# Kernel tuning notes

Measured on AMD Instinct MI355X. Metric: run time of the kernel, lower is better.

Reference implementation:

```python
import jax, jax.numpy as jnp
import numpy as np

THRESHOLD = 1.5
MIN_AREA = 3
B, H, W = 8, 1024, 1024


def _label_components(mask):
    """8-connectivity connected-component labeling by min-index propagation.
    mask: [B,H,W] bool. Returns int32 labels [B,H,W]; each component is labeled
    by the minimum global flat index of its pixels; background pixels = B*H*W.
    Labels are globally unique across the batch (matches sort_labels' per-batch
    unique relabeling up to a label permutation).
    """
    N = B * H * W
    SENT = jnp.int32(N)
    flat = jnp.arange(N, dtype=jnp.int32).reshape(B, H, W)
    lab0 = jnp.where(mask, flat, SENT)

    def neighbor_min(lab):
        p = jnp.pad(lab, ((0, 0), (1, 1), (1, 1)), constant_values=N)
        m = lab
        for dr in (-1, 0, 1):
            for dc in (-1, 0, 1):
                if dr == 0 and dc == 0:
                    continue
                m = jnp.minimum(m, p[:, 1 + dr:1 + dr + H, 1 + dc:1 + dc + W])
        return jnp.where(mask, m, SENT)

    def cond(state):
        return state[1]

    def body(state):
        lab, _ = state
        new = neighbor_min(lab)
        return new, jnp.any(new != lab)

    lab, _ = jax.lax.while_loop(cond, body, (lab0, jnp.array(True)))
    return lab


def setup_inputs() -> dict:
    key = jax.random.key(0)
    x = jax.random.normal(key, (B, H, W // 1), dtype=jnp.float32)
    return {"input_tensor": x.reshape(B, 1, H, W)}


def reference(input_tensor):
    """Dense encoding of the original ragged output: for every pixel belonging
    to a cluster with area > MIN_AREA, emit the cluster's max value and the
    (row, col) of the first (lowest flat index) occurrence of that max;
    background / small-cluster pixels get (0, -1, -1). Since THRESHOLD > 0,
    max over masked_fill(0) in the original equals max over cluster pixels.
    """
    x = input_tensor[:, 0]                  # [B,H,W]
    N = B * H * W
    nseg = N + 1                            # last segment = background
    mask = (x >= THRESHOLD)
    ids = _label_components(mask).reshape(-1)          # [N] int32 in [0, N]
    vals = x.reshape(-1)
    fg = mask.reshape(-1)

    area = jax.ops.segment_sum(fg.astype(jnp.float32), ids, num_segments=nseg)
    cmax = jax.ops.segment_max(vals, ids, num_segments=nseg)

    within = jnp.tile(jnp.arange(H * W, dtype=jnp.int32), B)  # flat idx in image
    is_max = (vals == cmax[ids]) & fg
    cand = jnp.where(is_max, within, jnp.int32(H * W))
    amin = jax.ops.segment_min(cand, ids, num_segments=nseg)  # first argmax

    valid = fg & (area[ids] > MIN_AREA)
    out_max = jnp.where(valid, cmax[ids], jnp.float32(0.0)).reshape(B, H, W)
    aidx = amin[ids]
    row = jnp.where(valid, aidx // W, jnp.int32(-1)).reshape(B, H, W)
    col = jnp.where(valid, aidx % W, jnp.int32(-1)).reshape(B, H, W)
    return out_max, row, col
```

## Files before the change

kernel.cpp:

```cpp
#include <hip/hip_runtime.h>
#include <stdint.h>

#define THRESH 1.5f
constexpr int NPIX  = 8 * 1024 * 1024;
constexpr int HW    = 1024 * 1024;
constexpr int WW    = 1024;
constexpr int NWORD = NPIX / 32;
constexpr int WPR   = WW / 32;

constexpr int BLK     = 256;
constexpr int GRD_PX4 = NPIX / (BLK * 4);
constexpr int GRD_W   = NWORD / BLK;

constexpr int SPB_R      = 128;
constexpr int BASE_SLOTS = GRD_PX4 * SPB_R;
constexpr int OVF_SLOTS  = 16384;
constexpr int CAP        = BASE_SLOTS + OVF_SLOTS;
constexpr int ZINT4 = CAP * 12 / 16;
static_assert((CAP * 12) % 16 == 0, "zero region must be int4-divisible");
static_assert(ZINT4 <= GRD_PX4 * BLK, "mask_init must cover the zero region");

constexpr int WLSTRIDE = 1024;


__device__ __forceinline__ int find_root(int* __restrict__ P, int x) {
    int p = P[x];
    while (p != x) {
        int g = P[p];
        if (g != p) P[x] = g;
        x = p; p = g;
    }
    return x;
}

__device__ __forceinline__ void merge(int* P, int a, int b) {
    int ra = find_root(P, a);
    int rb = find_root(P, b);
    while (ra != rb) {
        if (ra < rb) { int t = ra; ra = rb; rb = t; }
        int old = atomicCAS(&P[ra], ra, rb);
        if (old == ra) break;
        ra = find_root(P, old);
        rb = find_root(P, rb);
    }
}

__global__ void mask_init_k(const float* __restrict__ x, int* __restrict__ parent,
                            unsigned* __restrict__ mask, uint2* __restrict__ wl,
                            int* __restrict__ wl_cnt, int4* __restrict__ zbase,
                            int* __restrict__ ovf) {
    __shared__ unsigned s_nib[BLK];
    __shared__ unsigned s_word[WPR];
    __shared__ int s_rank;
    int t  = threadIdx.x;
    int gt = blockIdx.x * BLK + t;
    if (gt < ZINT4) zbase[gt] = make_int4(0, 0, 0, 0);
    int i4 = gt * 4;
    float4 v = *(const float4*)(x + i4);
    unsigned nib = (unsigned)(v.x >= THRESH) | ((unsigned)(v.y >= THRESH) << 1) |
                   ((unsigned)(v.z >= THRESH) << 2) | ((unsigned)(v.w >= THRESH) << 3);
    if (t == 0) s_rank = 0;
    s_nib[t] = nib;
    __syncthreads();
    if ((t & 7) == 0) {
        unsigned w = 0;
        #pragma unroll
        for (int k = 0; k < 8; k++) w |= s_nib[t + k] << (4 * k);
        s_word[t >> 3] = w;
        mask[gt >> 3] = w;
    }
    __syncthreads();

    int rowstart = blockIdx.x << 10;
    int r0 = t << 2;
    int rs0 = 0, rs1 = 0, rs2 = 0, rs3 = 0;
    if (nib & 1u) {
        bool prevSet = (r0 != 0) &&
            ((s_word[(r0 - 1) >> 5] >> ((r0 - 1) & 31)) & 1u);
        if (!prevSet) rs0 = r0;
        else {
            int wI = r0 >> 5, b = r0 & 31;
            unsigned notset = b ? (~s_word[wI] & ((1u << b) - 1)) : 0u;
            int j = wI;
            if (!notset) {
                j = wI - 1;
                while (j >= 0 && s_word[j] == 0xFFFFFFFFu) j--;
                notset = (j >= 0) ? ~s_word[j] : 0u;
            }
            rs0 = (j < 0) ? 0 : (j * 32 + (31 - __clz(notset)) + 1);
        }
    }
    if (nib & 2u) rs1 = (nib & 1u) ? rs0 : r0 + 1;
    if (nib & 4u) rs2 = (nib & 2u) ? rs1 : r0 + 2;
    if (nib & 8u) rs3 = (nib & 4u) ? rs2 : r0 + 3;
    int4 pv;
    pv.x = (nib & 1u) ? rowstart + rs0 : i4;
    pv.y = (nib & 2u) ? rowstart + rs1 : i4 + 1;
    pv.z = (nib & 4u) ? rowstart + rs2 : i4 + 2;
    pv.w = (nib & 8u) ? rowstart + rs3 : i4 + 3;
    *(int4*)(parent + i4) = pv;

    int nfg = __popc(nib);
    if (nfg) {
        int r = atomicAdd(&s_rank, nfg);
        uint2* dst = wl + (size_t)blockIdx.x * WLSTRIDE;
        if (nib & 1u) dst[r++] = make_uint2((unsigned)i4,     __float_as_uint(v.x));
        if (nib & 2u) dst[r++] = make_uint2((unsigned)i4 + 1, __float_as_uint(v.y));
        if (nib & 4u) dst[r++] = make_uint2((unsigned)i4 + 2, __float_as_uint(v.z));
        if (nib & 8u) dst[r++] = make_uint2((unsigned)i4 + 3, __float_as_uint(v.w));
    }
    __syncthreads();
    if (t == 0) wl_cnt[blockIdx.x] = s_rank;
    if (gt == 0) *ovf = 0;
}

__global__ void union_k(const unsigned* __restrict__ mask, int* __restrict__ parent) {
    int w = blockIdx.x * BLK + threadIdx.x;
    int r = (w >> 5) & (WW - 1);
    if (r == 0) return;
    unsigned cur = mask[w];
    if (!cur) return;
    int cw = w & (WPR - 1);
    unsigned above     = mask[w - WPR];
    unsigned abovePrev = (cw > 0)       ? mask[w - WPR - 1] : 0u;
    unsigned aboveNext = (cw < WPR - 1) ? mask[w - WPR + 1] : 0u;
    unsigned mN  = cur & above;
    unsigned mNW = cur & ((above << 1) | (abovePrev >> 31));
    unsigned mNE = cur & ((above >> 1) | ((aboveNext & 1u) << 31));
    mNW &= ~mN;
    mNE &= ~mN;
    mN  &= ~(mN << 1);
    if (!(mN | mNW | mNE)) return;
    int base = w << 5;
    while (mN)  { int b = __ffs(mN)  - 1; mN  &= mN  - 1; merge(parent, base + b, base + b - WW); }
    while (mNW) { int b = __ffs(mNW) - 1; mNW &= mNW - 1; merge(parent, base + b, base + b - WW - 1); }
    while (mNE) { int b = __ffs(mNE) - 1; mNE &= mNE - 1; merge(parent, base + b, base + b - WW + 1); }
}

__global__ void cstats_k(const uint2* __restrict__ wl, const int* __restrict__ wl_cnt,
                         int* __restrict__ parent, int* __restrict__ cnt,
                         unsigned long long* __restrict__ best,
                         int* __restrict__ ovf) {
    __shared__ int s_cnt;
    if (threadIdx.x == 0) s_cnt = 0;
    __syncthreads();
    int region = blockIdx.x;
    int c = wl_cnt[region];
    const uint2* src = wl + (size_t)region * WLSTRIDE;
    for (int j = threadIdx.x; j < c; j += 64) {
        uint2 e = src[j];
        int p = (int)e.x;
        int cid;
        int xn = p;
        while (true) {
            int pe = parent[xn];
            if (pe >= NPIX) { cid = pe - NPIX; break; }
            if (pe == xn) {
                int rank = atomicAdd(&s_cnt, 1);
                int slot;
                if (rank < SPB_R) slot = region * SPB_R + rank;
                else { int o2 = atomicAdd(ovf, 1);
                       slot = BASE_SLOTS + (o2 < OVF_SLOTS ? o2 : OVF_SLOTS - 1); }
                int old = atomicCAS(&parent[xn], xn, NPIX + slot);
                if (old == xn)    { cid = slot; break; }
                if (old >= NPIX)  { cid = old - NPIX; break; }
                xn = old;
            } else {
                xn = pe;
            }
        }
        parent[p] = NPIX + cid;
        atomicAdd(&cnt[cid], 1);
        unsigned within = (unsigned)(p & (HW - 1));
        unsigned long long pk =
            ((unsigned long long)e.y << 32) | (unsigned long long)(~within);
        atomicMax(&best[cid], pk);
    }
}

__device__ __forceinline__ void lookup_one(const int* __restrict__ parent,
                                           const int* __restrict__ cnt,
                                           const unsigned long long* __restrict__ best,
                                           int p, float& om, float& orow, float& ocol) {
    int cid = parent[p] - NPIX;
    if (cid >= 0 && cid < CAP && cnt[cid] > 3) {
        unsigned long long pk = best[cid];
        om   = __uint_as_float((unsigned)(pk >> 32));
        unsigned idx = ~((unsigned)pk);
        orow = (float)(idx >> 10);
        ocol = (float)(idx & (WW - 1));
    }
}

__global__ void out_k(const unsigned* __restrict__ mask, const int* __restrict__ parent,
                      const int* __restrict__ cnt,
                      const unsigned long long* __restrict__ best,
                      float* __restrict__ o) {
    int t = blockIdx.x * BLK + threadIdx.x;
    unsigned nib = (mask[t >> 3] >> ((t & 7) * 4)) & 0xFu;
    int i4 = t * 4;
    float4 m  = make_float4(0.f, 0.f, 0.f, 0.f);
    float4 rr = make_float4(-1.f, -1.f, -1.f, -1.f);
    float4 cc = make_float4(-1.f, -1.f, -1.f, -1.f);
    if (nib) {
        if (nib & 1u) lookup_one(parent, cnt, best, i4,     m.x, rr.x, cc.x);
        if (nib & 2u) lookup_one(parent, cnt, best, i4 + 1, m.y, rr.y, cc.y);
        if (nib & 4u) lookup_one(parent, cnt, best, i4 + 2, m.z, rr.z, cc.z);
        if (nib & 8u) lookup_one(parent, cnt, best, i4 + 3, m.w, rr.w, cc.w);
    }
    *(float4*)(o + i4)            = m;
    *(float4*)(o + NPIX + i4)     = rr;
    *(float4*)(o + 2 * NPIX + i4) = cc;
}

extern "C" void kernel_launch(void* const* d_in, const int* in_sizes, int n_in,
                              void* d_out, int out_size, void* d_ws, size_t ws_size,
                              hipStream_t stream) {
    const float* x = (const float*)d_in[0];
    float* o = (float*)d_out;

    char* base = (char*)d_ws;
    int* parent = (int*)base;
    size_t off = (size_t)NPIX * 4;
    unsigned long long* best = (unsigned long long*)(base + off);
    int4* zbase = (int4*)(base + off);                             off += (size_t)CAP * 8;
    int* cnt       = (int*)(base + off);                           off += (size_t)CAP * 4;
    unsigned* mask = (unsigned*)(base + off);                      off += (size_t)NWORD * 4;
    int* wl_cnt    = (int*)(base + off);                           off += (size_t)GRD_PX4 * 4;
    uint2* wl      = (uint2*)(base + off);                         off += (size_t)GRD_PX4 * WLSTRIDE * 8;
    int* ovf       = (int*)(base + off);

    mask_init_k<<<GRD_PX4, BLK, 0, stream>>>(x, parent, mask, wl, wl_cnt, zbase, ovf);
    union_k    <<<GRD_W,   BLK, 0, stream>>>(mask, parent);
    cstats_k   <<<GRD_PX4, 64,  0, stream>>>(wl, wl_cnt, parent, cnt, best, ovf);
    out_k      <<<GRD_PX4, BLK, 0, stream>>>(mask, parent, cnt, best, o);
}
```

Measured before the change: 189.7 us.

## Write default outputs in mask init and scatter cluster stats via worklist

The background default values (0,-1,-1) are now written in the first kernel while it already streams the input. The final full-image output pass is replaced by a sparse kernel that walks each block's foreground worklist and scatters stats only for foreground pixels. The cluster id is stored back into the worklist instead of parent, and parent writes are skipped for background-only threads. This removes a full read of mask and parent plus a dense gather pass, at the cost of scattered scalar stores and a 64-thread sparse launch.

```diff
diff --git a/kernel.cpp b/kernel.cpp
--- a/kernel.cpp
+++ b/kernel.cpp
@@ -48,7 +48,7 @@
 __global__ void mask_init_k(const float* __restrict__ x, int* __restrict__ parent,
                             unsigned* __restrict__ mask, uint2* __restrict__ wl,
                             int* __restrict__ wl_cnt, int4* __restrict__ zbase,
-                            int* __restrict__ ovf) {
+                            int* __restrict__ ovf, float* __restrict__ o) {
     __shared__ unsigned s_nib[BLK];
     __shared__ unsigned s_word[WPR];
     __shared__ int s_rank;
@@ -59,6 +59,10 @@
     float4 v = *(const float4*)(x + i4);
     unsigned nib = (unsigned)(v.x >= THRESH) | ((unsigned)(v.y >= THRESH) << 1) |
                    ((unsigned)(v.z >= THRESH) << 2) | ((unsigned)(v.w >= THRESH) << 3);
+    const float4 neg1 = make_float4(-1.f, -1.f, -1.f, -1.f);
+    *(float4*)(o + i4)            = make_float4(0.f, 0.f, 0.f, 0.f);
+    *(float4*)(o + NPIX + i4)     = neg1;
+    *(float4*)(o + 2 * NPIX + i4) = neg1;
     if (t == 0) s_rank = 0;
     s_nib[t] = nib;
     __syncthreads();
@@ -71,37 +75,37 @@
     }
     __syncthreads();
 
-    int rowstart = blockIdx.x << 10;
-    int r0 = t << 2;
-    int rs0 = 0, rs1 = 0, rs2 = 0, rs3 = 0;
-    if (nib & 1u) {
-        bool prevSet = (r0 != 0) &&
-            ((s_word[(r0 - 1) >> 5] >> ((r0 - 1) & 31)) & 1u);
-        if (!prevSet) rs0 = r0;
-        else {
-            int wI = r0 >> 5, b = r0 & 31;
-            unsigned notset = b ? (~s_word[wI] & ((1u << b) - 1)) : 0u;
-            int j = wI;
-            if (!notset) {
-                j = wI - 1;
-                while (j >= 0 && s_word[j] == 0xFFFFFFFFu) j--;
-                notset = (j >= 0) ? ~s_word[j] : 0u;
+    if (nib) {
+        int rowstart = blockIdx.x << 10;
+        int r0 = t << 2;
+        int rs0 = 0, rs1 = 0, rs2 = 0, rs3 = 0;
+        if (nib & 1u) {
+            bool prevSet = (r0 != 0) &&
+                ((s_word[(r0 - 1) >> 5] >> ((r0 - 1) & 31)) & 1u);
+            if (!prevSet) rs0 = r0;
+            else {
+                int wI = r0 >> 5, b = r0 & 31;
+                unsigned notset = b ? (~s_word[wI] & ((1u << b) - 1)) : 0u;
+                int j = wI;
+                if (!notset) {
+                    j = wI - 1;
+                    while (j >= 0 && s_word[j] == 0xFFFFFFFFu) j--;
+                    notset = (j >= 0) ? ~s_word[j] : 0u;
+                }
+                rs0 = (j < 0) ? 0 : (j * 32 + (31 - __clz(notset)) + 1);
             }
-            rs0 = (j < 0) ? 0 : (j * 32 + (31 - __clz(notset)) + 1);
         }
-    }
-    if (nib & 2u) rs1 = (nib & 1u) ? rs0 : r0 + 1;
-    if (nib & 4u) rs2 = (nib & 2u) ? rs1 : r0 + 2;
-    if (nib & 8u) rs3 = (nib & 4u) ? rs2 : r0 + 3;
-    int4 pv;
-    pv.x = (nib & 1u) ? rowstart + rs0 : i4;
-    pv.y = (nib & 2u) ? rowstart + rs1 : i4 + 1;
-    pv.z = (nib & 4u) ? rowstart + rs2 : i4 + 2;
-    pv.w = (nib & 8u) ? rowstart + rs3 : i4 + 3;
-    *(int4*)(parent + i4) = pv;
-
-    int nfg = __popc(nib);
-    if (nfg) {
+        if (nib & 2u) rs1 = (nib & 1u) ? rs0 : r0 + 1;
+        if (nib & 4u) rs2 = (nib & 2u) ? rs1 : r0 + 2;
+        if (nib & 8u) rs3 = (nib & 4u) ? rs2 : r0 + 3;
+        int4 pv;
+        pv.x = (nib & 1u) ? rowstart + rs0 : i4;
+        pv.y = (nib & 2u) ? rowstart + rs1 : i4 + 1;
+        pv.z = (nib & 4u) ? rowstart + rs2 : i4 + 2;
+        pv.w = (nib & 8u) ? rowstart + rs3 : i4 + 3;
+        *(int4*)(parent + i4) = pv;
+
+        int nfg = __popc(nib);
         int r = atomicAdd(&s_rank, nfg);
         uint2* dst = wl + (size_t)blockIdx.x * WLSTRIDE;
         if (nib & 1u) dst[r++] = make_uint2((unsigned)i4,     __float_as_uint(v.x));
@@ -137,7 +141,7 @@
     while (mNE) { int b = __ffs(mNE) - 1; mNE &= mNE - 1; merge(parent, base + b, base + b - WW + 1); }
 }
 
-__global__ void cstats_k(const uint2* __restrict__ wl, const int* __restrict__ wl_cnt,
+__global__ void cstats_k(uint2* __restrict__ wl, const int* __restrict__ wl_cnt,
                          int* __restrict__ parent, int* __restrict__ cnt,
                          unsigned long long* __restrict__ best,
                          int* __restrict__ ovf) {
@@ -146,7 +150,7 @@
     __syncthreads();
     int region = blockIdx.x;
     int c = wl_cnt[region];
-    const uint2* src = wl + (size_t)region * WLSTRIDE;
+    uint2* src = wl + (size_t)region * WLSTRIDE;
     for (int j = threadIdx.x; j < c; j += 64) {
         uint2 e = src[j];
         int p = (int)e.x;
@@ -169,7 +173,7 @@
                 xn = pe;
             }
         }
-        parent[p] = NPIX + cid;
+        src[j] = make_uint2(e.x, (unsigned)cid);
         atomicAdd(&cnt[cid], 1);
         unsigned within = (unsigned)(p & (HW - 1));
         unsigned long long pk =
@@ -178,39 +182,26 @@
     }
 }
 
-__device__ __forceinline__ void lookup_one(const int* __restrict__ parent,
-                                           const int* __restrict__ cnt,
-                                           const unsigned long long* __restrict__ best,
-                                           int p, float& om, float& orow, float& ocol) {
-    int cid = parent[p] - NPIX;
-    if (cid >= 0 && cid < CAP && cnt[cid] > 3) {
-        unsigned long long pk = best[cid];
-        om   = __uint_as_float((unsigned)(pk >> 32));
-        unsigned idx = ~((unsigned)pk);
-        orow = (float)(idx >> 10);
-        ocol = (float)(idx & (WW - 1));
-    }
-}
-
-__global__ void out_k(const unsigned* __restrict__ mask, const int* __restrict__ parent,
-                      const int* __restrict__ cnt,
-                      const unsigned long long* __restrict__ best,
-                      float* __restrict__ o) {
-    int t = blockIdx.x * BLK + threadIdx.x;
-    unsigned nib = (mask[t >> 3] >> ((t & 7) * 4)) & 0xFu;
-    int i4 = t * 4;
-    float4 m  = make_float4(0.f, 0.f, 0.f, 0.f);
-    float4 rr = make_float4(-1.f, -1.f, -1.f, -1.f);
-    float4 cc = make_float4(-1.f, -1.f, -1.f, -1.f);
-    if (nib) {
-        if (nib & 1u) lookup_one(parent, cnt, best, i4,     m.x, rr.x, cc.x);
-        if (nib & 2u) lookup_one(parent, cnt, best, i4 + 1, m.y, rr.y, cc.y);
-        if (nib & 4u) lookup_one(parent, cnt, best, i4 + 2, m.z, rr.z, cc.z);
-        if (nib & 8u) lookup_one(parent, cnt, best, i4 + 3, m.w, rr.w, cc.w);
-    }
-    *(float4*)(o + i4)            = m;
-    *(float4*)(o + NPIX + i4)     = rr;
-    *(float4*)(o + 2 * NPIX + i4) = cc;
+__global__ void sval_k(const uint2* __restrict__ wl, const int* __restrict__ wl_cnt,
+                       const int* __restrict__ cnt,
+                       const unsigned long long* __restrict__ best,
+                       float* __restrict__ o) {
+    int region = blockIdx.x;
+    int c = wl_cnt[region];
+    const uint2* src = wl + (size_t)region * WLSTRIDE;
+    for (int j = threadIdx.x; j < c; j += 64) {
+        uint2 e = src[j];
+        int p   = (int)e.x;
+        int cid = (int)e.y;
+        if (cid < 0 || cid >= CAP) continue;
+        if (cnt[cid] > 3) {
+            unsigned long long pk = best[cid];
+            unsigned idx = ~((unsigned)pk);
+            o[p]            = __uint_as_float((unsigned)(pk >> 32));
+            o[NPIX + p]     = (float)(idx >> 10);
+            o[2 * NPIX + p] = (float)(idx & (WW - 1));
+        }
+    }
 }
 
 extern "C" void kernel_launch(void* const* d_in, const int* in_sizes, int n_in,
@@ -230,8 +221,8 @@
     uint2* wl      = (uint2*)(base + off);                         off += (size_t)GRD_PX4 * WLSTRIDE * 8;
     int* ovf       = (int*)(base + off);
 
-    mask_init_k<<<GRD_PX4, BLK, 0, stream>>>(x, parent, mask, wl, wl_cnt, zbase, ovf);
+    mask_init_k<<<GRD_PX4, BLK, 0, stream>>>(x, parent, mask, wl, wl_cnt, zbase, ovf, o);
     union_k    <<<GRD_W,   BLK, 0, stream>>>(mask, parent);
     cstats_k   <<<GRD_PX4, 64,  0, stream>>>(wl, wl_cnt, parent, cnt, best, ovf);
-    out_k      <<<GRD_PX4, BLK, 0, stream>>>(mask, parent, cnt, best, o);
-}
+    sval_k     <<<GRD_PX4, 64,  0, stream>>>(wl, wl_cnt, cnt, best, o);
+}
```

New measurement: 197.3 us. 4.0% more time.

## Fuse intra-stripe row unions into mask init, union only stripe boundaries

Applied to the files above, without the earlier changes.

The mask/init kernel now processes 8-row stripes per block, keeps the stripe's bitmask words in shared memory, and performs the vertical unions between rows inside the stripe directly. A separate lightweight kernel then unions only the first row of each stripe with the row above. cstats now packs four 64-thread wavefronts per block, each handling one row region. This cuts global mask re-reads and launch work for the union pass, but gives fewer, longer-running blocks in the init kernel, with many barriers per block.

```diff
diff --git a/kernel.cpp b/kernel.cpp
--- a/kernel.cpp
+++ b/kernel.cpp
@@ -8,17 +8,19 @@
 constexpr int NWORD = NPIX / 32;
 constexpr int WPR   = WW / 32;
 
-constexpr int BLK     = 256;
-constexpr int GRD_PX4 = NPIX / (BLK * 4);
-constexpr int GRD_W   = NWORD / BLK;
+constexpr int BLK      = 256;
+constexpr int NROWS    = NPIX / WW;
+constexpr int SROWS    = 8;
+constexpr int NSTRIPE  = NROWS / SROWS;
+constexpr int GRD_PX4  = NPIX / (BLK * 4);
+constexpr int GRD_BU   = (NSTRIPE * WPR) / BLK;
 
 constexpr int SPB_R      = 128;
-constexpr int BASE_SLOTS = GRD_PX4 * SPB_R;
+constexpr int BASE_SLOTS = NROWS * SPB_R;
 constexpr int OVF_SLOTS  = 16384;
 constexpr int CAP        = BASE_SLOTS + OVF_SLOTS;
 constexpr int ZINT4 = CAP * 12 / 16;
 static_assert((CAP * 12) % 16 == 0, "zero region must be int4-divisible");
-static_assert(ZINT4 <= GRD_PX4 * BLK, "mask_init must cover the zero region");
 
 constexpr int WLSTRIDE = 1024;
 
@@ -45,109 +47,135 @@
     }
 }
 
-__global__ void mask_init_k(const float* __restrict__ x, int* __restrict__ parent,
-                            unsigned* __restrict__ mask, uint2* __restrict__ wl,
-                            int* __restrict__ wl_cnt, int4* __restrict__ zbase,
-                            int* __restrict__ ovf) {
-    __shared__ unsigned s_nib[BLK];
-    __shared__ unsigned s_word[WPR];
-    __shared__ int s_rank;
-    int t  = threadIdx.x;
-    int gt = blockIdx.x * BLK + t;
-    if (gt < ZINT4) zbase[gt] = make_int4(0, 0, 0, 0);
-    int i4 = gt * 4;
-    float4 v = *(const float4*)(x + i4);
-    unsigned nib = (unsigned)(v.x >= THRESH) | ((unsigned)(v.y >= THRESH) << 1) |
-                   ((unsigned)(v.z >= THRESH) << 2) | ((unsigned)(v.w >= THRESH) << 3);
-    if (t == 0) s_rank = 0;
-    s_nib[t] = nib;
-    __syncthreads();
-    if ((t & 7) == 0) {
-        unsigned w = 0;
-        #pragma unroll
-        for (int k = 0; k < 8; k++) w |= s_nib[t + k] << (4 * k);
-        s_word[t >> 3] = w;
-        mask[gt >> 3] = w;
-    }
-    __syncthreads();
-
-    int rowstart = blockIdx.x << 10;
-    int r0 = t << 2;
-    int rs0 = 0, rs1 = 0, rs2 = 0, rs3 = 0;
-    if (nib & 1u) {
-        bool prevSet = (r0 != 0) &&
-            ((s_word[(r0 - 1) >> 5] >> ((r0 - 1) & 31)) & 1u);
-        if (!prevSet) rs0 = r0;
-        else {
-            int wI = r0 >> 5, b = r0 & 31;
-            unsigned notset = b ? (~s_word[wI] & ((1u << b) - 1)) : 0u;
-            int j = wI;
-            if (!notset) {
-                j = wI - 1;
-                while (j >= 0 && s_word[j] == 0xFFFFFFFFu) j--;
-                notset = (j >= 0) ? ~s_word[j] : 0u;
-            }
-            rs0 = (j < 0) ? 0 : (j * 32 + (31 - __clz(notset)) + 1);
-        }
-    }
-    if (nib & 2u) rs1 = (nib & 1u) ? rs0 : r0 + 1;
-    if (nib & 4u) rs2 = (nib & 2u) ? rs1 : r0 + 2;
-    if (nib & 8u) rs3 = (nib & 4u) ? rs2 : r0 + 3;
-    int4 pv;
-    pv.x = (nib & 1u) ? rowstart + rs0 : i4;
-    pv.y = (nib & 2u) ? rowstart + rs1 : i4 + 1;
-    pv.z = (nib & 4u) ? rowstart + rs2 : i4 + 2;
-    pv.w = (nib & 8u) ? rowstart + rs3 : i4 + 3;
-    *(int4*)(parent + i4) = pv;
-
-    int nfg = __popc(nib);
-    if (nfg) {
-        int r = atomicAdd(&s_rank, nfg);
-        uint2* dst = wl + (size_t)blockIdx.x * WLSTRIDE;
-        if (nib & 1u) dst[r++] = make_uint2((unsigned)i4,     __float_as_uint(v.x));
-        if (nib & 2u) dst[r++] = make_uint2((unsigned)i4 + 1, __float_as_uint(v.y));
-        if (nib & 4u) dst[r++] = make_uint2((unsigned)i4 + 2, __float_as_uint(v.z));
-        if (nib & 8u) dst[r++] = make_uint2((unsigned)i4 + 3, __float_as_uint(v.w));
-    }
-    __syncthreads();
-    if (t == 0) wl_cnt[blockIdx.x] = s_rank;
-    if (gt == 0) *ovf = 0;
-}
-
-__global__ void union_k(const unsigned* __restrict__ mask, int* __restrict__ parent) {
-    int w = blockIdx.x * BLK + threadIdx.x;
-    int r = (w >> 5) & (WW - 1);
-    if (r == 0) return;
-    unsigned cur = mask[w];
-    if (!cur) return;
-    int cw = w & (WPR - 1);
-    unsigned above     = mask[w - WPR];
-    unsigned abovePrev = (cw > 0)       ? mask[w - WPR - 1] : 0u;
-    unsigned aboveNext = (cw < WPR - 1) ? mask[w - WPR + 1] : 0u;
+__device__ __forceinline__ void union_words(int* __restrict__ parent, int base,
+                                            unsigned cur, unsigned above,
+                                            unsigned abovePrev, unsigned aboveNext) {
     unsigned mN  = cur & above;
     unsigned mNW = cur & ((above << 1) | (abovePrev >> 31));
     unsigned mNE = cur & ((above >> 1) | ((aboveNext & 1u) << 31));
     mNW &= ~mN;
     mNE &= ~mN;
     mN  &= ~(mN << 1);
-    if (!(mN | mNW | mNE)) return;
-    int base = w << 5;
     while (mN)  { int b = __ffs(mN)  - 1; mN  &= mN  - 1; merge(parent, base + b, base + b - WW); }
     while (mNW) { int b = __ffs(mNW) - 1; mNW &= mNW - 1; merge(parent, base + b, base + b - WW - 1); }
     while (mNE) { int b = __ffs(mNE) - 1; mNE &= mNE - 1; merge(parent, base + b, base + b - WW + 1); }
+}
+
+__global__ void mask_init_k(const float* __restrict__ x, int* __restrict__ parent,
+                            unsigned* __restrict__ mask, uint2* __restrict__ wl,
+                            int* __restrict__ wl_cnt, int4* __restrict__ zbase,
+                            int* __restrict__ ovf) {
+    __shared__ unsigned s_nib[BLK];
+    __shared__ unsigned s_word[SROWS][WPR];
+    __shared__ int s_rank;
+    int t      = threadIdx.x;
+    int stripe = blockIdx.x;
+    for (int z = stripe * BLK + t; z < ZINT4; z += NSTRIPE * BLK)
+        zbase[z] = make_int4(0, 0, 0, 0);
+    if (stripe == 0 && t == 0) *ovf = 0;
+
+    int stripePix = stripe * (SROWS * WW);
+    for (int r = 0; r < SROWS; ++r) {
+        int rowstart = stripePix + r * WW;
+        int i4 = rowstart + t * 4;
+        float4 v = *(const float4*)(x + i4);
+        unsigned nib = (unsigned)(v.x >= THRESH) | ((unsigned)(v.y >= THRESH) << 1) |
+                       ((unsigned)(v.z >= THRESH) << 2) | ((unsigned)(v.w >= THRESH) << 3);
+        __syncthreads();
+        if (t == 0) s_rank = 0;
+        s_nib[t] = nib;
+        __syncthreads();
+        if ((t & 7) == 0) {
+            unsigned w = 0;
+            #pragma unroll
+            for (int k = 0; k < 8; k++) w |= s_nib[t + k] << (4 * k);
+            s_word[r][t >> 3] = w;
+            mask[i4 >> 5] = w;
+        }
+        __syncthreads();
+
+        if (nib) {
+            int r0 = t << 2;
+            int rs0 = 0, rs1 = 0, rs2 = 0, rs3 = 0;
+            if (nib & 1u) {
+                bool prevSet = (r0 != 0) &&
+                    ((s_word[r][(r0 - 1) >> 5] >> ((r0 - 1) & 31)) & 1u);
+                if (!prevSet) rs0 = r0;
+                else {
+                    int wI = r0 >> 5, b = r0 & 31;
+                    unsigned notset = b ? (~s_word[r][wI] & ((1u << b) - 1)) : 0u;
+                    int j = wI;
+                    if (!notset) {
+                        j = wI - 1;
+                        while (j >= 0 && s_word[r][j] == 0xFFFFFFFFu) j--;
+                        notset = (j >= 0) ? ~s_word[r][j] : 0u;
+                    }
+                    rs0 = (j < 0) ? 0 : (j * 32 + (31 - __clz(notset)) + 1);
+                }
+            }
+            if (nib & 2u) rs1 = (nib & 1u) ? rs0 : r0 + 1;
+            if (nib & 4u) rs2 = (nib & 2u) ? rs1 : r0 + 2;
+            if (nib & 8u) rs3 = (nib & 4u) ? rs2 : r0 + 3;
+            int4 pv;
+            pv.x = (nib & 1u) ? rowstart + rs0 : i4;
+            pv.y = (nib & 2u) ? rowstart + rs1 : i4 + 1;
+            pv.z = (nib & 4u) ? rowstart + rs2 : i4 + 2;
+            pv.w = (nib & 8u) ? rowstart + rs3 : i4 + 3;
+            *(int4*)(parent + i4) = pv;
+
+            int nfg = __popc(nib);
+            int rk = atomicAdd(&s_rank, nfg);
+            uint2* dst = wl + (size_t)(stripe * SROWS + r) * WLSTRIDE;
+            if (nib & 1u) dst[rk++] = make_uint2((unsigned)i4,     __float_as_uint(v.x));
+            if (nib & 2u) dst[rk++] = make_uint2((unsigned)i4 + 1, __float_as_uint(v.y));
+            if (nib & 4u) dst[rk++] = make_uint2((unsigned)i4 + 2, __float_as_uint(v.z));
+            if (nib & 8u) dst[rk++] = make_uint2((unsigned)i4 + 3, __float_as_uint(v.w));
+        }
+        __syncthreads();
+        if (t == 0) wl_cnt[stripe * SROWS + r] = s_rank;
+    }
+    __syncthreads();
+
+    if (t < (SROWS - 1) * WPR) {
+        int rl = 1 + (t >> 5);
+        int cw = t & 31;
+        unsigned cur = s_word[rl][cw];
+        if (cur) {
+            unsigned above     = s_word[rl - 1][cw];
+            unsigned abovePrev = (cw > 0)       ? s_word[rl - 1][cw - 1] : 0u;
+            unsigned aboveNext = (cw < WPR - 1) ? s_word[rl - 1][cw + 1] : 0u;
+            int base = stripePix + rl * WW + cw * 32;
+            union_words(parent, base, cur, above, abovePrev, aboveNext);
+        }
+    }
+}
+
+__global__ void b_union_k(const unsigned* __restrict__ mask, int* __restrict__ parent) {
+    int tid = blockIdx.x * BLK + threadIdx.x;
+    int s   = tid >> 5;
+    int cw  = tid & 31;
+    if ((s & 127) == 0) return;
+    int w = s * (SROWS * WPR) + cw;
+    unsigned cur = mask[w];
+    if (!cur) return;
+    unsigned above     = mask[w - WPR];
+    unsigned abovePrev = (cw > 0)       ? mask[w - WPR - 1] : 0u;
+    unsigned aboveNext = (cw < WPR - 1) ? mask[w - WPR + 1] : 0u;
+    union_words(parent, w << 5, cur, above, abovePrev, aboveNext);
 }
 
 __global__ void cstats_k(const uint2* __restrict__ wl, const int* __restrict__ wl_cnt,
                          int* __restrict__ parent, int* __restrict__ cnt,
                          unsigned long long* __restrict__ best,
                          int* __restrict__ ovf) {
-    __shared__ int s_cnt;
-    if (threadIdx.x == 0) s_cnt = 0;
+    __shared__ int s_cnt[4];
+    int t = threadIdx.x, ws = t >> 6, lane = t & 63;
+    if (lane == 0) s_cnt[ws] = 0;
     __syncthreads();
-    int region = blockIdx.x;
+    int region = blockIdx.x * 4 + ws;
     int c = wl_cnt[region];
     const uint2* src = wl + (size_t)region * WLSTRIDE;
-    for (int j = threadIdx.x; j < c; j += 64) {
+    for (int j = lane; j < c; j += 64) {
         uint2 e = src[j];
         int p = (int)e.x;
         int cid;
@@ -156,7 +184,7 @@
             int pe = parent[xn];
             if (pe >= NPIX) { cid = pe - NPIX; break; }
             if (pe == xn) {
-                int rank = atomicAdd(&s_cnt, 1);
+                int rank = atomicAdd(&s_cnt[ws], 1);
                 int slot;
                 if (rank < SPB_R) slot = region * SPB_R + rank;
                 else { int o2 = atomicAdd(ovf, 1);
@@ -226,12 +254,12 @@
     int4* zbase = (int4*)(base + off);                             off += (size_t)CAP * 8;
     int* cnt       = (int*)(base + off);                           off += (size_t)CAP * 4;
     unsigned* mask = (unsigned*)(base + off);                      off += (size_t)NWORD * 4;
-    int* wl_cnt    = (int*)(base + off);                           off += (size_t)GRD_PX4 * 4;
-    uint2* wl      = (uint2*)(base + off);                         off += (size_t)GRD_PX4 * WLSTRIDE * 8;
+    int* wl_cnt    = (int*)(base + off);                           off += (size_t)NROWS * 4;
+    uint2* wl      = (uint2*)(base + off);                         off += (size_t)NROWS * WLSTRIDE * 8;
     int* ovf       = (int*)(base + off);
 
-    mask_init_k<<<GRD_PX4, BLK, 0, stream>>>(x, parent, mask, wl, wl_cnt, zbase, ovf);
-    union_k    <<<GRD_W,   BLK, 0, stream>>>(mask, parent);
-    cstats_k   <<<GRD_PX4, 64,  0, stream>>>(wl, wl_cnt, parent, cnt, best, ovf);
+    mask_init_k<<<NSTRIPE, BLK, 0, stream>>>(x, parent, mask, wl, wl_cnt, zbase, ovf);
+    b_union_k  <<<GRD_BU,  BLK, 0, stream>>>(mask, parent);
+    cstats_k   <<<2048,    BLK, 0, stream>>>(wl, wl_cnt, parent, cnt, best, ovf);
     out_k      <<<GRD_PX4, BLK, 0, stream>>>(mask, parent, cnt, best, o);
 }
```

Result: slower. 207.9 us (+9.6%).
